# Kernel optimization log

Hardware: AMD Instinct MI355X
Metric: run time of the kernel (lower is better)

The kernel has to match this reference:

```python
import jax, jax.numpy as jnp
import numpy as np

# Gate hyperparameters (from init_kwargs)
DIM = 4096
N_EXPERTS = 256        # n_routed_experts
N_GROUPS = 8           # n_expert_groups
TOPK_GROUPS = 4        # n_limited_groups
TOPK = 8               # n_activated_experts
ROUTE_SCALE = 1.0
N_TOKENS = 16384       # batch * seq_len flattened


def setup_inputs() -> dict:
    key = jax.random.key(0)
    kx, kw = jax.random.split(key)
    x = jax.random.normal(kx, (N_TOKENS, DIM), dtype=jnp.float32)
    # xavier-ish scale for the gate projection weight [n_experts, dim]
    weight = jax.random.normal(kw, (N_EXPERTS, DIM), dtype=jnp.float32) * (1.0 / np.sqrt(DIM))
    return {"x": x, "weight": weight}


def reference(x, weight):
    T = x.shape[0]
    # scores = linear(x, weight)  -> [T, E]
    logits = jnp.einsum('td,ed->te', x, weight)
    # score_func == 'softmax' computed in fp32 (torch: softmax(dim=-1, dtype=float32))
    scores = jax.nn.softmax(logits.astype(jnp.float32), axis=-1)
    original_scores = scores

    # group-limited routing (n_groups > 1, no bias -> amax per group)
    sg = scores.reshape(T, N_GROUPS, N_EXPERTS // N_GROUPS)   # [T, G, E/G]
    group_scores = jnp.max(sg, axis=-1)                        # [T, G]
    _, gidx = jax.lax.top_k(group_scores, TOPK_GROUPS)         # [T, topk_groups]
    keep = jnp.zeros((T, N_GROUPS), dtype=bool)
    keep = keep.at[jnp.arange(T)[:, None], gidx].set(True)
    masked = jnp.where(keep[:, :, None], sg, -jnp.inf).reshape(T, N_EXPERTS)

    # top-k expert selection; weights gathered from the un-masked scores
    _, idx = jax.lax.top_k(masked, TOPK)                       # [T, topk]
    weights = jnp.take_along_axis(original_scores, idx, axis=1)
    weights = weights * ROUTE_SCALE
    return weights.astype(x.dtype), idx
```

## Files before the change

### kernel.cpp

```cpp
#include <hip/hip_runtime.h>
#include <math.h>
#include <stdint.h>

#define NTOK   16384
#define DIM    4096
#define NEXP   256
#define TOPKG  4
#define TOPK   8
#define NSPLIT 4
#define KCHUNK (DIM / NSPLIT)
#define BM     128
#define BK     32
#define NSTEPS (KCHUNK / BK)

typedef float v4f   __attribute__((ext_vector_type(4)));
typedef short short8 __attribute__((ext_vector_type(8)));

__device__ inline unsigned short f2bf(float x) {
    unsigned u = __float_as_uint(x);
    return (unsigned short)((u + 0x7fffu + ((u >> 16) & 1u)) >> 16);
}
__device__ inline float bf2f(unsigned short h) {
    return __uint_as_float(((unsigned)h) << 16);
}
__device__ inline int swz4(int row, int slot) { return slot ^ ((row >> 1) & 3); }

__global__ __launch_bounds__(256) void wprep(const float* __restrict__ W,
                                             unsigned short* __restrict__ Wh,
                                             unsigned short* __restrict__ Wl) {
    int i = (blockIdx.x * 256 + threadIdx.x) * 4;
    float4 v = *(const float4*)(W + i);
    ushort4 h, l;
    h.x = f2bf(v.x); l.x = f2bf(v.x - bf2f(h.x));
    h.y = f2bf(v.y); l.y = f2bf(v.y - bf2f(h.y));
    h.z = f2bf(v.z); l.z = f2bf(v.z - bf2f(h.z));
    h.w = f2bf(v.w); l.w = f2bf(v.w - bf2f(h.w));
    *(ushort4*)(Wh + i) = h;
    *(ushort4*)(Wl + i) = l;
}

__global__ __launch_bounds__(256, 2) void gate_gemm(const float* __restrict__ X,
                                                    const unsigned short* __restrict__ Wh,
                                                    const unsigned short* __restrict__ Wl,
                                                    float* __restrict__ P) {
    __shared__ __align__(16) unsigned short Ah[2][BM * BK];
    __shared__ __align__(16) unsigned short Al[2][BM * BK];

    const int t  = threadIdx.x;
    const int bm = blockIdx.x * BM;
    const int z  = blockIdx.y;
    const int k0 = z * KCHUNK;

    const int l  = t & 63;
    const int wc = t >> 6;
    const int lm = l & 15;
    const int lq = l >> 4;

    const int ar = t >> 1;
    const float* xrow = X + (size_t)(bm + ar) * DIM + k0 + (t & 1) * 16;

    const unsigned short* bsrc_h[4];
    const unsigned short* bsrc_l[4];
#pragma unroll
    for (int c = 0; c < 4; ++c) {
        int e = wc * 64 + c * 16 + lm;
        bsrc_h[c] = Wh + (size_t)e * DIM + k0 + lq * 8;
        bsrc_l[c] = Wl + (size_t)e * DIM + k0 + lq * 8;
    }

#define ACONV(buf, v0, v1, v2, v3)                                                  \
    do {                                                                            \
        float4 xa_[4] = {v0, v1, v2, v3};                                           \
        _Pragma("unroll")                                                           \
        for (int i_ = 0; i_ < 4; ++i_) {                                            \
            ushort4 h_, lo_;                                                        \
            h_.x = f2bf(xa_[i_].x); lo_.x = f2bf(xa_[i_].x - bf2f(h_.x));           \
            h_.y = f2bf(xa_[i_].y); lo_.y = f2bf(xa_[i_].y - bf2f(h_.y));           \
            h_.z = f2bf(xa_[i_].z); lo_.z = f2bf(xa_[i_].z - bf2f(h_.z));           \
            h_.w = f2bf(xa_[i_].w); lo_.w = f2bf(xa_[i_].w - bf2f(h_.w));           \
            int j_ = (t & 1) * 4 + i_;                                              \
            int idx_ = ar * BK + swz4(ar, j_ >> 1) * 8 + (j_ & 1) * 4;              \
            *(ushort4*)&Ah[buf][idx_] = h_;                                         \
            *(ushort4*)&Al[buf][idx_] = lo_;                                        \
        }                                                                           \
    } while (0)

#define LOADB(dsth, dstl, step)                                                     \
    do {                                                                            \
        _Pragma("unroll")                                                           \
        for (int c_ = 0; c_ < 4; ++c_) {                                            \
            dsth[c_] = *(const short8*)(bsrc_h[c_] + (step) * BK);                  \
            dstl[c_] = *(const short8*)(bsrc_l[c_] + (step) * BK);                  \
        }                                                                           \
    } while (0)

    v4f acc[8][4] = {};
    short8 bAh[4], bAl[4], bBh[4], bBl[4];
    float4 xv0, xv1, xv2, xv3;

    {
        float4 p0 = *(const float4*)(xrow);
        float4 p1 = *(const float4*)(xrow + 4);
        float4 p2 = *(const float4*)(xrow + 8);
        float4 p3 = *(const float4*)(xrow + 12);
        LOADB(bAh, bAl, 0);
        ACONV(0, p0, p1, p2, p3);
        asm volatile("s_waitcnt lgkmcnt(0)" ::: "memory");
        __builtin_amdgcn_s_barrier();
    }

    int cur = 0;
#define STEP(s, bch, bcl, bnh, bnl)                                                 \
    do {                                                                            \
        const bool pf_ = ((s) + 1 < NSTEPS);                                        \
        if (pf_) {                                                                  \
            const float* xn_ = xrow + ((s) + 1) * BK;                               \
            xv0 = *(const float4*)(xn_);                                            \
            xv1 = *(const float4*)(xn_ + 4);                                        \
            xv2 = *(const float4*)(xn_ + 8);                                        \
            xv3 = *(const float4*)(xn_ + 12);                                       \
            LOADB(bnh, bnl, (s) + 1);                                               \
        }                                                                           \
        __builtin_amdgcn_s_setprio(1);                                              \
        _Pragma("unroll")                                                           \
        for (int r_ = 0; r_ < 8; ++r_) {                                            \
            const int m_ = r_ * 16 + lm;                                            \
            short8 ah_ = *(const short8*)&Ah[cur][m_ * BK + swz4(m_, lq) * 8];      \
            short8 al_ = *(const short8*)&Al[cur][m_ * BK + swz4(m_, lq) * 8];      \
            _Pragma("unroll")                                                       \
            for (int c_ = 0; c_ < 4; ++c_) {                                        \
                acc[r_][c_] = __builtin_amdgcn_mfma_f32_16x16x32_bf16(ah_, bch[c_], acc[r_][c_], 0, 0, 0); \
                acc[r_][c_] = __builtin_amdgcn_mfma_f32_16x16x32_bf16(ah_, bcl[c_], acc[r_][c_], 0, 0, 0); \
                acc[r_][c_] = __builtin_amdgcn_mfma_f32_16x16x32_bf16(al_, bch[c_], acc[r_][c_], 0, 0, 0); \
            }                                                                       \
        }                                                                           \
        __builtin_amdgcn_s_setprio(0);                                              \
        if (pf_) ACONV(cur ^ 1, xv0, xv1, xv2, xv3);                                \
        asm volatile("s_waitcnt lgkmcnt(0)" ::: "memory");                          \
        __builtin_amdgcn_s_barrier();                                               \
        cur ^= 1;                                                                   \
    } while (0)

#pragma unroll 1
    for (int s2 = 0; s2 < NSTEPS; s2 += 2) {
        STEP(s2,     bAh, bAl, bBh, bBl);
        STEP(s2 + 1, bBh, bBl, bAh, bAl);
    }
#undef STEP
#undef LOADB
#undef ACONV

    float* Pb = P + ((size_t)z * NTOK + bm) * NEXP;
#pragma unroll
    for (int r = 0; r < 8; ++r)
#pragma unroll
        for (int c = 0; c < 4; ++c)
#pragma unroll
            for (int g = 0; g < 4; ++g)
                Pb[(size_t)(r * 16 + lq * 4 + g) * NEXP + wc * 64 + c * 16 + lm] = acc[r][c][g];
}

__global__ __launch_bounds__(256) void gate_route(const float* __restrict__ P,
                                                  float* __restrict__ outw,
                                                  float* __restrict__ outi) {
    const int lane = threadIdx.x & 63;
    const int tok  = (blockIdx.x * blockDim.x + threadIdx.x) >> 6;
    if (tok >= NTOK) return;

    float l[4] = {0.f, 0.f, 0.f, 0.f};
#pragma unroll
    for (int z = 0; z < NSPLIT; ++z) {
        float4 v = *(const float4*)(P + ((size_t)z * NTOK + tok) * NEXP + lane * 4);
        l[0] += v.x; l[1] += v.y; l[2] += v.z; l[3] += v.w;
    }

    float lmax = fmaxf(fmaxf(l[0], l[1]), fmaxf(l[2], l[3]));
    float m = lmax;
#pragma unroll
    for (int o = 32; o; o >>= 1) m = fmaxf(m, __shfl_xor(m, o));

    float s = __expf(l[0] - m) + __expf(l[1] - m) + __expf(l[2] - m) + __expf(l[3] - m);
#pragma unroll
    for (int o = 32; o; o >>= 1) s += __shfl_xor(s, o);

    float gm = lmax;
#pragma unroll
    for (int o = 4; o; o >>= 1) gm = fmaxf(gm, __shfl_xor(gm, o));

    const int g = lane >> 3;
    int rank = 0;
#pragma unroll
    for (int gg = 0; gg < 8; ++gg) {
        float vg = __shfl(gm, gg * 8);
        rank += (vg > gm) || (vg == gm && gg < g);
    }
    const bool allowed = rank < TOPKG;

    float mv[4];
#pragma unroll
    for (int j = 0; j < 4; ++j) mv[j] = allowed ? l[j] : -INFINITY;

    float wsel = 0.0f;
    int   isel = 0;

    for (int k = 0; k < TOPK; ++k) {
        float bv = mv[0];
        int   bi = lane * 4;
        if (mv[1] > bv) { bv = mv[1]; bi = lane * 4 + 1; }
        if (mv[2] > bv) { bv = mv[2]; bi = lane * 4 + 2; }
        if (mv[3] > bv) { bv = mv[3]; bi = lane * 4 + 3; }
#pragma unroll
        for (int o = 32; o; o >>= 1) {
            float ov = __shfl_xor(bv, o);
            int   oi = __shfl_xor(bi, o);
            if (ov > bv || (ov == bv && oi < bi)) { bv = ov; bi = oi; }
        }
        if (lane == k) { wsel = __expf(bv - m) / s; isel = bi; }
        if ((bi >> 2) == lane) mv[bi & 3] = -INFINITY;
    }

    if (lane < TOPK) {
        outw[(size_t)tok * TOPK + lane] = wsel;
        outi[(size_t)tok * TOPK + lane] = (float)isel;
    }
}

extern "C" void kernel_launch(void* const* d_in, const int* in_sizes, int n_in,
                              void* d_out, int out_size, void* d_ws, size_t ws_size,
                              hipStream_t stream) {
    const float* x  = (const float*)d_in[0];
    const float* wt = (const float*)d_in[1];

    float* P = (float*)d_ws;
    unsigned short* Wh = (unsigned short*)((char*)d_ws + (size_t)NSPLIT * NTOK * NEXP * 4);
    unsigned short* Wl = Wh + (size_t)NEXP * DIM;

    float* outw = (float*)d_out;
    float* outi = (float*)d_out + (size_t)NTOK * TOPK;

    wprep<<<(NEXP * DIM) / (256 * 4), 256, 0, stream>>>(wt, Wh, Wl);

    dim3 ggrid(NTOK / BM, NSPLIT);
    gate_gemm<<<ggrid, 256, 0, stream>>>(x, Wh, Wl, P);

    gate_route<<<(NTOK * 64) / 256, 256, 0, stream>>>(P, outw, outi);
}
```

Measured before the change: 448.6 us.

## Stage X tiles into LDS via async global_load_lds with two-deep prefetch

Replaces the register-staged fp32 X loads with direct global-to-LDS async loads into a new double-buffered fp32 LDS buffer (XOR-swizzled). The bf16 hi/lo split then reads from LDS, and X is prefetched two steps ahead so global latency overlaps the MFMA work. This frees VGPRs held for prefetched X and deepens the pipeline. In exchange it adds 32KB of LDS per block, which may reduce occupancy at 2 blocks per CU, and relies on a hand-written vmcnt wait count being correct.

```diff
diff --git a/kernel.cpp b/kernel.cpp
--- a/kernel.cpp
+++ b/kernel.cpp
@@ -43,6 +43,7 @@
                                                     const unsigned short* __restrict__ Wh,
                                                     const unsigned short* __restrict__ Wl,
                                                     float* __restrict__ P) {
+    __shared__ __align__(16) float          Xf[2][BM * BK];
     __shared__ __align__(16) unsigned short Ah[2][BM * BK];
     __shared__ __align__(16) unsigned short Al[2][BM * BK];
 
@@ -57,7 +58,15 @@
     const int lq = l >> 4;
 
     const int ar = t >> 1;
-    const float* xrow = X + (size_t)(bm + ar) * DIM + k0 + (t & 1) * 16;
+    const int h  = t & 1;
+
+    const float* xg[4];
+#pragma unroll
+    for (int i = 0; i < 4; ++i) {
+        int flat = i * 256 + t;
+        int xr = flat >> 3, xs = flat & 7;
+        xg[i] = X + (size_t)(bm + xr) * DIM + k0 + ((xs ^ (xr & 7)) << 2);
+    }
 
     const unsigned short* bsrc_h[4];
     const unsigned short* bsrc_l[4];
@@ -68,9 +77,34 @@
         bsrc_l[c] = Wl + (size_t)e * DIM + k0 + lq * 8;
     }
 
-#define ACONV(buf, v0, v1, v2, v3)                                                  \
-    do {                                                                            \
-        float4 xa_[4] = {v0, v1, v2, v3};                                           \
+#define XSTAGE(R, step)                                                             \
+    do {                                                                            \
+        _Pragma("unroll")                                                           \
+        for (int i_ = 0; i_ < 4; ++i_) {                                            \
+            int flat_ = i_ * 256 + t;                                               \
+            __builtin_amdgcn_global_load_lds(                                       \
+                (const __attribute__((address_space(1))) unsigned int*)(xg[i_] + (step) * BK), \
+                (__attribute__((address_space(3))) unsigned int*)&Xf[R][flat_ * 4], 16, 0, 0); \
+        }                                                                           \
+    } while (0)
+
+#define LOADB(dsth, dstl, step)                                                     \
+    do {                                                                            \
+        _Pragma("unroll")                                                           \
+        for (int c_ = 0; c_ < 4; ++c_) {                                            \
+            dsth[c_] = *(const short8*)(bsrc_h[c_] + (step) * BK);                  \
+            dstl[c_] = *(const short8*)(bsrc_l[c_] + (step) * BK);                  \
+        }                                                                           \
+    } while (0)
+
+#define CONV(R)                                                                     \
+    do {                                                                            \
+        float4 xa_[4];                                                              \
+        _Pragma("unroll")                                                           \
+        for (int j_ = 0; j_ < 4; ++j_) {                                            \
+            int phys_ = (h * 4 + j_) ^ (ar & 7);                                    \
+            xa_[j_] = *(const float4*)&Xf[R][ar * 32 + phys_ * 4];                  \
+        }                                                                           \
         _Pragma("unroll")                                                           \
         for (int i_ = 0; i_ < 4; ++i_) {                                            \
             ushort4 h_, lo_;                                                        \
@@ -78,55 +112,20 @@
             h_.y = f2bf(xa_[i_].y); lo_.y = f2bf(xa_[i_].y - bf2f(h_.y));           \
             h_.z = f2bf(xa_[i_].z); lo_.z = f2bf(xa_[i_].z - bf2f(h_.z));           \
             h_.w = f2bf(xa_[i_].w); lo_.w = f2bf(xa_[i_].w - bf2f(h_.w));           \
-            int j_ = (t & 1) * 4 + i_;                                              \
+            int j_ = h * 4 + i_;                                                    \
             int idx_ = ar * BK + swz4(ar, j_ >> 1) * 8 + (j_ & 1) * 4;              \
-            *(ushort4*)&Ah[buf][idx_] = h_;                                         \
-            *(ushort4*)&Al[buf][idx_] = lo_;                                        \
-        }                                                                           \
-    } while (0)
-
-#define LOADB(dsth, dstl, step)                                                     \
-    do {                                                                            \
-        _Pragma("unroll")                                                           \
-        for (int c_ = 0; c_ < 4; ++c_) {                                            \
-            dsth[c_] = *(const short8*)(bsrc_h[c_] + (step) * BK);                  \
-            dstl[c_] = *(const short8*)(bsrc_l[c_] + (step) * BK);                  \
-        }                                                                           \
-    } while (0)
-
-    v4f acc[8][4] = {};
-    short8 bAh[4], bAl[4], bBh[4], bBl[4];
-    float4 xv0, xv1, xv2, xv3;
-
-    {
-        float4 p0 = *(const float4*)(xrow);
-        float4 p1 = *(const float4*)(xrow + 4);
-        float4 p2 = *(const float4*)(xrow + 8);
-        float4 p3 = *(const float4*)(xrow + 12);
-        LOADB(bAh, bAl, 0);
-        ACONV(0, p0, p1, p2, p3);
-        asm volatile("s_waitcnt lgkmcnt(0)" ::: "memory");
-        __builtin_amdgcn_s_barrier();
-    }
-
-    int cur = 0;
-#define STEP(s, bch, bcl, bnh, bnl)                                                 \
-    do {                                                                            \
-        const bool pf_ = ((s) + 1 < NSTEPS);                                        \
-        if (pf_) {                                                                  \
-            const float* xn_ = xrow + ((s) + 1) * BK;                               \
-            xv0 = *(const float4*)(xn_);                                            \
-            xv1 = *(const float4*)(xn_ + 4);                                        \
-            xv2 = *(const float4*)(xn_ + 8);                                        \
-            xv3 = *(const float4*)(xn_ + 12);                                       \
-            LOADB(bnh, bnl, (s) + 1);                                               \
-        }                                                                           \
-        __builtin_amdgcn_s_setprio(1);                                              \
+            *(ushort4*)&Ah[R][idx_] = h_;                                           \
+            *(ushort4*)&Al[R][idx_] = lo_;                                          \
+        }                                                                           \
+    } while (0)
+
+#define MM(Pc, bch, bcl)                                                            \
+    do {                                                                            \
         _Pragma("unroll")                                                           \
         for (int r_ = 0; r_ < 8; ++r_) {                                            \
             const int m_ = r_ * 16 + lm;                                            \
-            short8 ah_ = *(const short8*)&Ah[cur][m_ * BK + swz4(m_, lq) * 8];      \
-            short8 al_ = *(const short8*)&Al[cur][m_ * BK + swz4(m_, lq) * 8];      \
+            short8 ah_ = *(const short8*)&Ah[Pc][m_ * BK + swz4(m_, lq) * 8];       \
+            short8 al_ = *(const short8*)&Al[Pc][m_ * BK + swz4(m_, lq) * 8];       \
             _Pragma("unroll")                                                       \
             for (int c_ = 0; c_ < 4; ++c_) {                                        \
                 acc[r_][c_] = __builtin_amdgcn_mfma_f32_16x16x32_bf16(ah_, bch[c_], acc[r_][c_], 0, 0, 0); \
@@ -134,21 +133,52 @@
                 acc[r_][c_] = __builtin_amdgcn_mfma_f32_16x16x32_bf16(al_, bch[c_], acc[r_][c_], 0, 0, 0); \
             }                                                                       \
         }                                                                           \
+    } while (0)
+
+    v4f acc[8][4] = {};
+    short8 bAh[4], bAl[4], bBh[4], bBl[4];
+
+    {
+        XSTAGE(0, 0);
+        XSTAGE(1, 1);
+        LOADB(bAh, bAl, 0);
+        asm volatile("s_waitcnt vmcnt(12)" ::: "memory");
+        __builtin_amdgcn_sched_barrier(0);
+        __builtin_amdgcn_s_barrier();
+        CONV(0);
+        asm volatile("s_waitcnt lgkmcnt(0)" ::: "memory");
+        __builtin_amdgcn_sched_barrier(0);
+        __builtin_amdgcn_s_barrier();
+    }
+
+#define STEP(s, Pc, bCh, bCl, bNh, bNl)                                             \
+    do {                                                                            \
+        if ((s) + 2 < NSTEPS) XSTAGE(Pc, (s) + 2);                                  \
+        if ((s) + 1 < NSTEPS) {                                                     \
+            LOADB(bNh, bNl, (s) + 1);                                               \
+            asm volatile("s_waitcnt vmcnt(12)" ::: "memory");                       \
+            __builtin_amdgcn_sched_barrier(0);                                      \
+        }                                                                           \
+        __builtin_amdgcn_s_barrier();              \
+        __builtin_amdgcn_s_setprio(1);                                              \
+        MM(Pc, bCh, bCl);                                                           \
         __builtin_amdgcn_s_setprio(0);                                              \
-        if (pf_) ACONV(cur ^ 1, xv0, xv1, xv2, xv3);                                \
+        if ((s) + 1 < NSTEPS) CONV(Pc ^ 1);       \
         asm volatile("s_waitcnt lgkmcnt(0)" ::: "memory");                          \
+        __builtin_amdgcn_sched_barrier(0);                                          \
         __builtin_amdgcn_s_barrier();                                               \
-        cur ^= 1;                                                                   \
     } while (0)
 
 #pragma unroll 1
     for (int s2 = 0; s2 < NSTEPS; s2 += 2) {
-        STEP(s2,     bAh, bAl, bBh, bBl);
-        STEP(s2 + 1, bBh, bBl, bAh, bAl);
+        STEP(s2,     0, bAh, bAl, bBh, bBl);
+        STEP(s2 + 1, 1, bBh, bBl, bAh, bAl);
     }
 #undef STEP
+#undef MM
+#undef CONV
 #undef LOADB
-#undef ACONV
+#undef XSTAGE
 
     float* Pb = P + ((size_t)z * NTOK + bm) * NEXP;
 #pragma unroll
```

After: 499.5 us. +11.4%, slower.
